# Kernel tuning notes

Measured on AMD Instinct MI355X. Metric: run time of the kernel, lower is better.

Reference implementation:

```python
import jax, jax.numpy as jnp
import numpy as np

N_NODES = 100000
N_EDGES = 1600000
D_IN = 128
D_OUT = 128


def setup_inputs() -> dict:
    key = jax.random.key(0)
    k1, k2, k3, k4, k5 = jax.random.split(key, 5)
    h = jax.random.normal(k1, (N_NODES, D_IN), dtype=jnp.float32)
    src = jax.random.randint(k2, (N_EDGES,), 0, N_NODES, dtype=jnp.int64)
    dst = jax.random.randint(k3, (N_EDGES,), 0, N_NODES, dtype=jnp.int64)
    # Glorot-ish init for linear weights (PyTorch nn.Linear style: [out, in])
    scale = 1.0 / np.sqrt(D_IN)
    W_self = jax.random.uniform(k4, (D_OUT, D_IN), jnp.float32, -scale, scale)
    W_neigh = jax.random.uniform(k5, (D_OUT, D_IN), jnp.float32, -scale, scale)
    b = jnp.zeros((D_OUT,), dtype=jnp.float32)
    return {"h": h, "src": src, "dst": dst, "W_self": W_self,
            "W_neigh": W_neigh, "b": b}


def reference(h, src, dst, W_self, W_neigh, b):
    n_nodes = h.shape[0]
    # neighbor gather + segment-mean over in-neighbors (DGL fn.copy_u + fn.mean)
    msg = h[src]                                            # [E, D_in]
    neigh_sum = jax.ops.segment_sum(msg, dst, num_segments=n_nodes)
    deg = jax.ops.segment_sum(jnp.ones_like(dst, dtype=h.dtype), dst,
                              num_segments=n_nodes)         # [N]
    h_neigh = neigh_sum / jnp.maximum(deg, 1.0)[:, None]    # mean; 0 for isolated
    # SAGEConv mean: fc_self(h) + fc_neigh(h_neigh) + bias
    out = h @ W_self.T + h_neigh @ W_neigh.T + b
    return out
```

## Files before the change

kernel.cpp:

```cpp
#include <hip/hip_runtime.h>
#include <stdint.h>

#define NN 100000
#define NE 1600000
#define DD 128
#define NTILES ((NN + 127) / 128)
#define NB 256
#define CHUNK (NE / NB)
#define NBUCK ((NN + 255) / 256)
#define GH_N (NBUCK * NB)
#define GH_BLK (GH_N / 256)

typedef __bf16 bf16x8 __attribute__((ext_vector_type(8)));
typedef float f32x4 __attribute__((ext_vector_type(4)));
typedef float f32x2 __attribute__((ext_vector_type(2)));

__device__ __forceinline__ unsigned int f2bf2(float a, float b) {
  union { float f; unsigned u; } x, y;
  x.f = a; y.f = b;
  unsigned ua = x.u + (0x7FFFu + ((x.u >> 16) & 1u));
  unsigned ub = y.u + (0x7FFFu + ((y.u >> 16) & 1u));
  return (ua >> 16) | (ub & 0xFFFF0000u);
}

__global__ __launch_bounds__(256) void convert_hist_kernel(
    const float4* __restrict__ hp, uint2* __restrict__ h8,
    const int* __restrict__ dst, int* __restrict__ gh) {
  __shared__ int lh[NBUCK];
  int gid = blockIdx.x * 256 + threadIdx.x;
  float4 a = hp[2 * gid], b = hp[2 * gid + 1];
  int lo = __builtin_amdgcn_cvt_pk_fp8_f32(a.x, a.y, 0, false);
  lo = __builtin_amdgcn_cvt_pk_fp8_f32(a.z, a.w, lo, true);
  int hi = __builtin_amdgcn_cvt_pk_fp8_f32(b.x, b.y, 0, false);
  hi = __builtin_amdgcn_cvt_pk_fp8_f32(b.z, b.w, hi, true);
  h8[gid] = make_uint2((unsigned)lo, (unsigned)hi);

  if (blockIdx.x < NB) {
    int t = threadIdx.x, bb = blockIdx.x;
    for (int i = t; i < NBUCK; i += 256) lh[i] = 0;
    __syncthreads();
    int e0 = bb * CHUNK;
    for (int e = e0 + t; e < e0 + CHUNK; e += 256)
      atomicAdd(&lh[dst[e] >> 8], 1);
    __syncthreads();
    for (int i = t; i < NBUCK; i += 256) gh[i * NB + bb] = lh[i];
  }
}

__global__ __launch_bounds__(256) void blocksum_kernel(const int* __restrict__ gh,
                                                       int* __restrict__ bsum) {
  __shared__ int s[256];
  int t = threadIdx.x;
  s[t] = gh[blockIdx.x * 256 + t];
  __syncthreads();
  for (int d = 128; d > 0; d >>= 1) {
    if (t < d) s[t] += s[t + d];
    __syncthreads();
  }
  if (t == 0) bsum[blockIdx.x] = s[0];
}

__global__ __launch_bounds__(512) void scanbsum_kernel(const int* __restrict__ bsum,
                                                       int* __restrict__ bsum_ex) {
  __shared__ int s[512];
  int t = threadIdx.x;
  int v = (t < GH_BLK) ? bsum[t] : 0;
  s[t] = v;
  __syncthreads();
  for (int d = 1; d < 512; d <<= 1) {
    int x = (t >= d) ? s[t - d] : 0;
    __syncthreads();
    s[t] += x;
    __syncthreads();
  }
  if (t < GH_BLK) bsum_ex[t] = s[t] - v;
}

__global__ __launch_bounds__(256) void scanfull_kernel(const int* __restrict__ gh,
                                                       const int* __restrict__ bsum_ex,
                                                       int* __restrict__ gsc) {
  __shared__ int s[256];
  int t = threadIdx.x;
  int idx = blockIdx.x * 256 + t;
  int v = gh[idx];
  s[t] = v;
  __syncthreads();
  for (int d = 1; d < 256; d <<= 1) {
    int x = (t >= d) ? s[t - d] : 0;
    __syncthreads();
    s[t] += x;
    __syncthreads();
  }
  gsc[idx] = bsum_ex[blockIdx.x] + s[t] - v;
}

__global__ __launch_bounds__(256) void coarse_scatter_kernel(
    const int* __restrict__ src, const int* __restrict__ dst,
    const int* __restrict__ gsc, unsigned* __restrict__ ebuf) {
  __shared__ int lhpad[512];
  __shared__ int lbase[NBUCK];
  __shared__ int lcur[NBUCK];
  __shared__ int gstart[NBUCK];
  __shared__ unsigned sdata[CHUNK];
  __shared__ int sgpos[CHUNK];
  int t = threadIdx.x, b = blockIdx.x;
  lhpad[t] = 0;
  lhpad[t + 256] = 0;
  __syncthreads();
  int e0 = b * CHUNK;
  for (int e = e0 + t; e < e0 + CHUNK; e += 256)
    atomicAdd(&lhpad[dst[e] >> 8], 1);
  __syncthreads();
  int cnt0 = lhpad[t], cnt1 = lhpad[t + 256];
  for (int d = 1; d < 512; d <<= 1) {
    int x0 = (t >= d) ? lhpad[t - d] : 0;
    int x1 = ((t + 256) >= d) ? lhpad[t + 256 - d] : 0;
    __syncthreads();
    lhpad[t] += x0;
    lhpad[t + 256] += x1;
    __syncthreads();
  }
  if (t < NBUCK) { lbase[t] = lhpad[t] - cnt0; lcur[t] = 0; gstart[t] = gsc[t * NB + b]; }
  int i2 = t + 256;
  if (i2 < NBUCK) { lbase[i2] = lhpad[i2] - cnt1; lcur[i2] = 0; gstart[i2] = gsc[i2 * NB + b]; }
  __syncthreads();
  for (int e = e0 + t; e < e0 + CHUNK; e += 256) {
    int d = dst[e], s = src[e];
    int bk = d >> 8;
    int slot = atomicAdd(&lcur[bk], 1);
    int lp = lbase[bk] + slot;
    sdata[lp] = ((unsigned)(d & 255) << 24) | (unsigned)s;
    sgpos[lp] = gstart[bk] + slot;
  }
  __syncthreads();
  for (int j = t; j < CHUNK; j += 256) ebuf[sgpos[j]] = sdata[j];
}

__global__ __launch_bounds__(256) void fine_sort_kernel(const unsigned* __restrict__ ebuf,
                                                        const int* __restrict__ gsc,
                                                        int* __restrict__ csr,
                                                        int* __restrict__ offs) {
  __shared__ int hist[256], scn[256], cur[256];
  int t = threadIdx.x, g = blockIdx.x;
  int base = gsc[g * NB];
  int end = (g == NBUCK - 1) ? NE : gsc[(g + 1) * NB];
  hist[t] = 0;
  __syncthreads();
  for (int j = base + t; j < end; j += 256)
    atomicAdd(&hist[ebuf[j] >> 24], 1);
  __syncthreads();
  int v = hist[t];
  scn[t] = v;
  __syncthreads();
  for (int d = 1; d < 256; d <<= 1) {
    int x = (t >= d) ? scn[t - d] : 0;
    __syncthreads();
    scn[t] += x;
    __syncthreads();
  }
  int excl = scn[t] - v;
  int node = g * 256 + t;
  if (node < NN) offs[node] = base + excl;
  if (node == NN - 1) offs[NN] = NE;
  cur[t] = excl;
  __syncthreads();
  for (int j = base + t; j < end; j += 256) {
    unsigned p = ebuf[j];
    int pos = atomicAdd(&cur[p >> 24], 1);
    csr[base + pos] = (int)(p & 0x00FFFFFFu);
  }
}

__device__ __forceinline__ void acc16(float* a, uint4 u) {
  f32x2 p;
  p = __builtin_amdgcn_cvt_pk_f32_fp8(u.x, false); a[0] += p.x;  a[1] += p.y;
  p = __builtin_amdgcn_cvt_pk_f32_fp8(u.x, true);  a[2] += p.x;  a[3] += p.y;
  p = __builtin_amdgcn_cvt_pk_f32_fp8(u.y, false); a[4] += p.x;  a[5] += p.y;
  p = __builtin_amdgcn_cvt_pk_f32_fp8(u.y, true);  a[6] += p.x;  a[7] += p.y;
  p = __builtin_amdgcn_cvt_pk_f32_fp8(u.z, false); a[8] += p.x;  a[9] += p.y;
  p = __builtin_amdgcn_cvt_pk_f32_fp8(u.z, true);  a[10] += p.x; a[11] += p.y;
  p = __builtin_amdgcn_cvt_pk_f32_fp8(u.w, false); a[12] += p.x; a[13] += p.y;
  p = __builtin_amdgcn_cvt_pk_f32_fp8(u.w, true);  a[14] += p.x; a[15] += p.y;
}

__device__ __forceinline__ void stage_f32(const float* __restrict__ X,
                                          int row0, int nvalid,
                                          uint4* buf, int t) {
#pragma unroll
  for (int i = 0; i < 8; i++) {
    int id = t + (i << 8);
    int r = id >> 4;
    int c8 = id & 15;
    int row = row0 + r;
    float4 v0 = {0.f, 0.f, 0.f, 0.f}, v1 = {0.f, 0.f, 0.f, 0.f};
    if (row < nvalid) {
      const float4* p = (const float4*)(X + (size_t)row * DD + (c8 << 3));
      v0 = p[0];
      v1 = p[1];
    }
    uint4 q;
    q.x = f2bf2(v0.x, v0.y);
    q.y = f2bf2(v0.z, v0.w);
    q.z = f2bf2(v1.x, v1.y);
    q.w = f2bf2(v1.z, v1.w);
    int rt = r >> 4, m = r & 15, kc = c8 >> 2, quad = c8 & 3;
    buf[(((rt << 2) + kc) << 6) + (quad << 4) + m] = q;
  }
}

__device__ __forceinline__ void compute_half(const uint4* sA, const uint4* sW,
                                             f32x4 acc[2][8], int wv, int lane) {
#pragma unroll
  for (int kc = 0; kc < 4; kc++) {
    bf16x8 b[8];
#pragma unroll
    for (int n = 0; n < 8; n++)
      b[n] = *(const bf16x8*)&sW[(((n << 2) + kc) << 6) + lane];
    bf16x8 a0 = *(const bf16x8*)&sA[((((wv * 2 + 0) << 2) + kc) << 6) + lane];
    bf16x8 a1 = *(const bf16x8*)&sA[((((wv * 2 + 1) << 2) + kc) << 6) + lane];
#pragma unroll
    for (int n = 0; n < 8; n++) {
      acc[0][n] = __builtin_amdgcn_mfma_f32_16x16x32_bf16(a0, b[n], acc[0][n], 0, 0, 0);
      acc[1][n] = __builtin_amdgcn_mfma_f32_16x16x32_bf16(a1, b[n], acc[1][n], 0, 0, 0);
    }
  }
}

__global__ __launch_bounds__(256, 2) void gemm_fused_kernel(
    const float* __restrict__ h, const uint4* __restrict__ h8,
    const int* __restrict__ offs, const int* __restrict__ csr,
    const float* __restrict__ Wself, const float* __restrict__ Wneigh,
    const float* __restrict__ bias, float* __restrict__ out) {
  __shared__ uint4 sA[2048];
  __shared__ uint4 sW[2048];
  int t = threadIdx.x;
  int wv = t >> 6;
  int lane = t & 63;
  int row0 = blockIdx.x * 128;

  f32x4 acc[2][8];
#pragma unroll
  for (int i = 0; i < 2; i++)
#pragma unroll
    for (int n = 0; n < 8; n++) acc[i][n] = f32x4{0.f, 0.f, 0.f, 0.f};

  stage_f32(h, row0, NN, sA, t);
  stage_f32(Wself, 0, 128, sW, t);
  __syncthreads();
  compute_half(sA, sW, acc, wv, lane);
  __syncthreads();

  stage_f32(Wneigh, 0, 128, sW, t);

  int grp = t >> 3;
  int l = t & 7;
#pragma unroll 1
  for (int rnd = 0; rnd < 4; rnd++) {
    int r = rnd * 32 + grp;
    int q = row0 + r;
    float a[16];
#pragma unroll
    for (int i = 0; i < 16; i++) a[i] = 0.f;
    float sc = 0.f;
    if (q < NN) {
      int off0 = offs[q], off1 = offs[q + 1];
      int j = off0;
      for (; j + 4 <= off1; j += 4) {
        int s0 = csr[j], s1 = csr[j + 1], s2 = csr[j + 2], s3 = csr[j + 3];
        uint4 u0 = h8[(size_t)s0 * 8 + l];
        uint4 u1 = h8[(size_t)s1 * 8 + l];
        uint4 u2 = h8[(size_t)s2 * 8 + l];
        uint4 u3 = h8[(size_t)s3 * 8 + l];
        acc16(a, u0); acc16(a, u1); acc16(a, u2); acc16(a, u3);
      }
      for (; j < off1; j++) acc16(a, h8[(size_t)csr[j] * 8 + l]);
      int deg = off1 - off0;
      sc = (deg > 0) ? (1.0f / (float)deg) : 0.0f;
    }
    uint4 r0, r1;
    r0.x = f2bf2(a[0] * sc, a[1] * sc);   r0.y = f2bf2(a[2] * sc, a[3] * sc);
    r0.z = f2bf2(a[4] * sc, a[5] * sc);   r0.w = f2bf2(a[6] * sc, a[7] * sc);
    r1.x = f2bf2(a[8] * sc, a[9] * sc);   r1.y = f2bf2(a[10] * sc, a[11] * sc);
    r1.z = f2bf2(a[12] * sc, a[13] * sc); r1.w = f2bf2(a[14] * sc, a[15] * sc);
    int rt = r >> 4, m = r & 15;
    int c8a = 2 * l, c8b = 2 * l + 1;
    sA[(((rt << 2) + (c8a >> 2)) << 6) + ((c8a & 3) << 4) + m] = r0;
    sA[(((rt << 2) + (c8b >> 2)) << 6) + ((c8b & 3) << 4) + m] = r1;
  }
  __syncthreads();
  compute_half(sA, sW, acc, wv, lane);

  int col = lane & 15, rq = lane >> 4;
  float bv[8];
#pragma unroll
  for (int n = 0; n < 8; n++) bv[n] = bias[n * 16 + col];
#pragma unroll
  for (int rt = 0; rt < 2; rt++) {
    int rb = row0 + (wv * 2 + rt) * 16 + rq * 4;
#pragma unroll
    for (int r = 0; r < 4; r++) {
      int row = rb + r;
      if (row < NN) {
        float* op = out + (size_t)row * DD + col;
#pragma unroll
        for (int n = 0; n < 8; n++) op[n * 16] = acc[rt][n][r] + bv[n];
      }
    }
  }
}

extern "C" void kernel_launch(void* const* d_in, const int* in_sizes, int n_in,
                              void* d_out, int out_size, void* d_ws, size_t ws_size,
                              hipStream_t stream) {
  const float* h      = (const float*)d_in[0];
  const int*   src    = (const int*)d_in[1];
  const int*   dst    = (const int*)d_in[2];
  const float* Wself  = (const float*)d_in[3];
  const float* Wneigh = (const float*)d_in[4];
  const float* bias   = (const float*)d_in[5];
  float* out = (float*)d_out;

  char* ws = (char*)d_ws;
  unsigned* h8       = (unsigned*)ws;
  unsigned* ebuf     = (unsigned*)(ws + 12800000);
  int*      csr      = (int*)(ws + 38400000);
  int*      gh       = (int*)(ws + 44800000);
  int*      gsc      = (int*)(ws + 45200384);
  int*      bsum     = (int*)(ws + 45600768);
  int*      bsum_ex  = (int*)(ws + 45602336);
  int*      offs     = (int*)(ws + 45603904);

  convert_hist_kernel<<<6250, 256, 0, stream>>>((const float4*)h, (uint2*)h8, dst, gh);
  blocksum_kernel<<<GH_BLK, 256, 0, stream>>>(gh, bsum);
  scanbsum_kernel<<<1, 512, 0, stream>>>(bsum, bsum_ex);
  scanfull_kernel<<<GH_BLK, 256, 0, stream>>>(gh, bsum_ex, gsc);
  coarse_scatter_kernel<<<NB, 256, 0, stream>>>(src, dst, gsc, ebuf);
  fine_sort_kernel<<<NBUCK, 256, 0, stream>>>(ebuf, gsc, csr, offs);
  gemm_fused_kernel<<<NTILES, 256, 0, stream>>>(h, (const uint4*)h8, offs, csr,
                                                Wself, Wneigh, bias, out);
}
```

Measured before the change: 234.2 us.

## Split neighbor gather into separate kernel writing MFMA-fragment layout

The neighbor mean gather moves out of the fused GEMM into its own kernel. That kernel uses a much larger grid (one 8-thread group per node) and writes bf16 results into a global buffer already laid out as MFMA A-fragments. The GEMM kernel then loads those fragments straight into registers, skipping the shared-memory staging for the neighbor half. The goal is more parallelism and latency hiding for the irregular gather, which was limited by the 2-block occupancy of the GEMM kernel. The cost is an extra launch plus a round trip of the bf16 fragment buffer through global memory.

Measured after the change: 224.1 us. 4.3% less time.

```diff
diff --git a/kernel.cpp b/kernel.cpp
--- a/kernel.cpp
+++ b/kernel.cpp
@@ -183,6 +183,44 @@
   p = __builtin_amdgcn_cvt_pk_f32_fp8(u.w, true);  a[14] += p.x; a[15] += p.y;
 }
 
+__global__ __launch_bounds__(256) void gather_frag_kernel(
+    const uint4* __restrict__ h8, const int* __restrict__ offs,
+    const int* __restrict__ csr, uint4* __restrict__ hfrag) {
+  int q = (blockIdx.x * 256 + threadIdx.x) >> 3;
+  int l = threadIdx.x & 7;
+  float a[16];
+#pragma unroll
+  for (int i = 0; i < 16; i++) a[i] = 0.f;
+  float sc = 0.f;
+  if (q < NN) {
+    int off0 = offs[q], off1 = offs[q + 1];
+    int j = off0;
+    for (; j + 4 <= off1; j += 4) {
+      int s0 = csr[j], s1 = csr[j + 1], s2 = csr[j + 2], s3 = csr[j + 3];
+      uint4 u0 = h8[(size_t)s0 * 8 + l];
+      uint4 u1 = h8[(size_t)s1 * 8 + l];
+      uint4 u2 = h8[(size_t)s2 * 8 + l];
+      uint4 u3 = h8[(size_t)s3 * 8 + l];
+      acc16(a, u0); acc16(a, u1); acc16(a, u2); acc16(a, u3);
+    }
+    for (; j < off1; j++) acc16(a, h8[(size_t)csr[j] * 8 + l]);
+    int deg = off1 - off0;
+    sc = (deg > 0) ? (1.0f / (float)deg) : 0.0f;
+  }
+  uint4 r0, r1;
+  r0.x = f2bf2(a[0] * sc, a[1] * sc);   r0.y = f2bf2(a[2] * sc, a[3] * sc);
+  r0.z = f2bf2(a[4] * sc, a[5] * sc);   r0.w = f2bf2(a[6] * sc, a[7] * sc);
+  r1.x = f2bf2(a[8] * sc, a[9] * sc);   r1.y = f2bf2(a[10] * sc, a[11] * sc);
+  r1.z = f2bf2(a[12] * sc, a[13] * sc); r1.w = f2bf2(a[14] * sc, a[15] * sc);
+  int r = q & 127;
+  int rt = r >> 4, m = r & 15;
+  int kc = l >> 1, quad = (l & 1) << 1;
+  int slot = (((rt << 2) + kc) << 6) + (quad << 4) + m;
+  uint4* base = hfrag + (size_t)(q >> 7) * 2048;
+  base[slot] = r0;
+  base[slot + 16] = r1;
+}
+
 __device__ __forceinline__ void stage_f32(const float* __restrict__ X,
                                           int row0, int nvalid,
                                           uint4* buf, int t) {
@@ -226,9 +264,8 @@
   }
 }
 
-__global__ __launch_bounds__(256, 2) void gemm_fused_kernel(
-    const float* __restrict__ h, const uint4* __restrict__ h8,
-    const int* __restrict__ offs, const int* __restrict__ csr,
+__global__ __launch_bounds__(256, 2) void gemm_kernel(
+    const float* __restrict__ h, const uint4* __restrict__ hfrag,
     const float* __restrict__ Wself, const float* __restrict__ Wneigh,
     const float* __restrict__ bias, float* __restrict__ out) {
   __shared__ uint4 sA[2048];
@@ -238,6 +275,14 @@
   int lane = t & 63;
   int row0 = blockIdx.x * 128;
 
+  const uint4* fb = hfrag + (size_t)blockIdx.x * 2048;
+  uint4 a2[8];
+#pragma unroll
+  for (int kc = 0; kc < 4; kc++) {
+    a2[kc]     = fb[((((wv * 2 + 0) << 2) + kc) << 6) + lane];
+    a2[4 + kc] = fb[((((wv * 2 + 1) << 2) + kc) << 6) + lane];
+  }
+
   f32x4 acc[2][8];
 #pragma unroll
   for (int i = 0; i < 2; i++)
@@ -251,44 +296,21 @@
   __syncthreads();
 
   stage_f32(Wneigh, 0, 128, sW, t);
-
-  int grp = t >> 3;
-  int l = t & 7;
-#pragma unroll 1
-  for (int rnd = 0; rnd < 4; rnd++) {
-    int r = rnd * 32 + grp;
-    int q = row0 + r;
-    float a[16];
-#pragma unroll
-    for (int i = 0; i < 16; i++) a[i] = 0.f;
-    float sc = 0.f;
-    if (q < NN) {
-      int off0 = offs[q], off1 = offs[q + 1];
-      int j = off0;
-      for (; j + 4 <= off1; j += 4) {
-        int s0 = csr[j], s1 = csr[j + 1], s2 = csr[j + 2], s3 = csr[j + 3];
-        uint4 u0 = h8[(size_t)s0 * 8 + l];
-        uint4 u1 = h8[(size_t)s1 * 8 + l];
-        uint4 u2 = h8[(size_t)s2 * 8 + l];
-        uint4 u3 = h8[(size_t)s3 * 8 + l];
-        acc16(a, u0); acc16(a, u1); acc16(a, u2); acc16(a, u3);
-      }
-      for (; j < off1; j++) acc16(a, h8[(size_t)csr[j] * 8 + l]);
-      int deg = off1 - off0;
-      sc = (deg > 0) ? (1.0f / (float)deg) : 0.0f;
-    }
-    uint4 r0, r1;
-    r0.x = f2bf2(a[0] * sc, a[1] * sc);   r0.y = f2bf2(a[2] * sc, a[3] * sc);
-    r0.z = f2bf2(a[4] * sc, a[5] * sc);   r0.w = f2bf2(a[6] * sc, a[7] * sc);
-    r1.x = f2bf2(a[8] * sc, a[9] * sc);   r1.y = f2bf2(a[10] * sc, a[11] * sc);
-    r1.z = f2bf2(a[12] * sc, a[13] * sc); r1.w = f2bf2(a[14] * sc, a[15] * sc);
-    int rt = r >> 4, m = r & 15;
-    int c8a = 2 * l, c8b = 2 * l + 1;
-    sA[(((rt << 2) + (c8a >> 2)) << 6) + ((c8a & 3) << 4) + m] = r0;
-    sA[(((rt << 2) + (c8b >> 2)) << 6) + ((c8b & 3) << 4) + m] = r1;
-  }
-  __syncthreads();
-  compute_half(sA, sW, acc, wv, lane);
+  __syncthreads();
+#pragma unroll
+  for (int kc = 0; kc < 4; kc++) {
+    bf16x8 b[8];
+#pragma unroll
+    for (int n = 0; n < 8; n++)
+      b[n] = *(const bf16x8*)&sW[(((n << 2) + kc) << 6) + lane];
+    bf16x8 a0 = *(const bf16x8*)&a2[kc];
+    bf16x8 a1 = *(const bf16x8*)&a2[4 + kc];
+#pragma unroll
+    for (int n = 0; n < 8; n++) {
+      acc[0][n] = __builtin_amdgcn_mfma_f32_16x16x32_bf16(a0, b[n], acc[0][n], 0, 0, 0);
+      acc[1][n] = __builtin_amdgcn_mfma_f32_16x16x32_bf16(a1, b[n], acc[1][n], 0, 0, 0);
+    }
+  }
 
   int col = lane & 15, rq = lane >> 4;
   float bv[8];
@@ -322,13 +344,14 @@
 
   char* ws = (char*)d_ws;
   unsigned* h8       = (unsigned*)ws;
+  unsigned* hfrag    = (unsigned*)(ws + 12800000);
   unsigned* ebuf     = (unsigned*)(ws + 12800000);
-  int*      csr      = (int*)(ws + 38400000);
-  int*      gh       = (int*)(ws + 44800000);
-  int*      gsc      = (int*)(ws + 45200384);
-  int*      bsum     = (int*)(ws + 45600768);
-  int*      bsum_ex  = (int*)(ws + 45602336);
-  int*      offs     = (int*)(ws + 45603904);
+  int*      csr      = (int*)(ws + 38425600);
+  int*      gh       = (int*)(ws + 44825600);
+  int*      gsc      = (int*)(ws + 45225984);
+  int*      bsum     = (int*)(ws + 45626368);
+  int*      bsum_ex  = (int*)(ws + 45627936);
+  int*      offs     = (int*)(ws + 45629504);
 
   convert_hist_kernel<<<6250, 256, 0, stream>>>((const float4*)h, (uint2*)h8, dst, gh);
   blocksum_kernel<<<GH_BLK, 256, 0, stream>>>(gh, bsum);
@@ -336,6 +359,8 @@
   scanfull_kernel<<<GH_BLK, 256, 0, stream>>>(gh, bsum_ex, gsc);
   coarse_scatter_kernel<<<NB, 256, 0, stream>>>(src, dst, gsc, ebuf);
   fine_sort_kernel<<<NBUCK, 256, 0, stream>>>(ebuf, gsc, csr, offs);
-  gemm_fused_kernel<<<NTILES, 256, 0, stream>>>(h, (const uint4*)h8, offs, csr,
-                                                Wself, Wneigh, bias, out);
-}
+  gather_frag_kernel<<<(NTILES * 128) / 32, 256, 0, stream>>>(
+      (const uint4*)h8, offs, csr, (uint4*)hfrag);
+  gemm_kernel<<<NTILES, 256, 0, stream>>>(h, (const uint4*)hfrag,
+                                          Wself, Wneigh, bias, out);
+}
```
